# Kernel optimization log

Measured on AMD Instinct MI355X. Metric: run time of the kernel, lower is better.

The kernel has to match this reference:

```python
import jax, jax.numpy as jnp
import numpy as np

B, T, M, L = 128, 500, 512, 128


def setup_inputs() -> dict:
    key = jax.random.key(0)
    ks = jax.random.split(key, 9)
    s = 0.05
    return {
        "H": jax.random.normal(ks[0], (B, T, M), jnp.float32),
        "Wv": jax.random.normal(ks[1], (M, L), jnp.float32) * s,
        "bv": jax.random.normal(ks[2], (L,), jnp.float32) * s,
        "Wu": jax.random.normal(ks[3], (M, L), jnp.float32) * s,
        "bu": jax.random.normal(ks[4], (L,), jnp.float32) * s,
        "Wa": jax.random.normal(ks[5], (L, 1), jnp.float32) * s,
        "ba": jax.random.normal(ks[6], (1,), jnp.float32) * s,
        "Wc": jax.random.normal(ks[7], (M, 2), jnp.float32) * s,
        "bc": jax.random.normal(ks[8], (2,), jnp.float32) * s,
    }


def reference(H, Wv, bv, Wu, bu, Wa, ba, Wc, bc):
    # Gated attention: tanh and sigmoid gates over per-tile features  [B,T,L]
    A_V = jnp.tanh(H @ Wv + bv)
    A_U = jax.nn.sigmoid(H @ Wu + bu)
    A = (A_V * A_U) @ Wa + ba            # [B,T,1]  (K=1)
    A_t = jnp.swapaxes(A, 1, 2)          # [B,1,T]  (transpose(2,1) in torch)
    # Per-bag softmax over tiles, replacing the Python loop with a batched op
    A_sm = jax.nn.softmax(A_t, axis=-1)  # [B,1,T]
    # Weighted sum of tile features per bag (batched mm replaces the loop+cat)
    Mpool = jnp.matmul(A_sm, H)          # [B,1,M]
    out = Mpool.reshape(B, M) @ Wc + bc  # [B,2]
    A_after_sftmx = A_sm.reshape(B, T)   # cat of [1,T] rows -> [B,T]
    # torch A.squeeze(0) with B>1 is a no-op -> [B,1,T]
    return (out, A_after_sftmx, A_t)
```

## Files before the change

### kernel.cpp

```cpp
#include <hip/hip_runtime.h>
#include <hip/hip_bf16.h>
#include <cstdint>

#define B_ 128
#define T_ 500
#define M_ 512
#define L_ 128
#define NTILE 8

typedef float  f32x4  __attribute__((ext_vector_type(4)));
typedef __bf16 bf16x8 __attribute__((ext_vector_type(8)));

__device__ __forceinline__ uint32_t f2bf(float f) {
  uint32_t u = __float_as_uint(f);
  u += 0x7FFFu + ((u >> 16) & 1u);
  return u >> 16;
}

__device__ __forceinline__ void gld_lds16(const uint16_t* g, uint16_t* l) {
  __builtin_amdgcn_global_load_lds((const __attribute__((address_space(1))) uint32_t*)g,
                                   (__attribute__((address_space(3))) uint32_t*)l,
                                   16, 0, 0);
}

__global__ void k_wconv(const float* __restrict__ Wv, const float* __restrict__ Wu,
                        uint16_t* __restrict__ Wb) {
  int id = blockIdx.x * 256 + threadIdx.x;
  int w = id >> 16;
  int r = id & 65535;
  int l = r >> 9;
  int m = r & 511;
  const float* src = w ? Wu : Wv;
  Wb[(w << 16) + l * 512 + m] = (uint16_t)f2bf(src[m * 128 + l]);
}

__global__ __launch_bounds__(256)
void k_gates_pool(const float* __restrict__ H, const uint16_t* __restrict__ Wb,
                  const float* __restrict__ bv, const float* __restrict__ bu,
                  const float* __restrict__ Wa, const float* __restrict__ ba,
                  float* __restrict__ At, float* __restrict__ Ew,
                  float* __restrict__ Sums, float* __restrict__ Mp8) {
  __shared__ __align__(16) uint16_t sm[20480];
  __shared__ float esm[64];
  const int tid  = threadIdx.x;
  const int lane = tid & 63;
  const int wv   = tid >> 6;
  const int lc   = lane & 15;
  const int kq   = lane >> 4;
  const int tile  = blockIdx.x;
  const int b     = blockIdx.y;
  const int tbase = tile * 64;

  const int ht  = tid >> 2;
  const int hcc = tid & 3;
  const int gts = tbase + ht;
  const bool hv = (gts < T_);
  const float* hsrc = H + ((size_t)b * T_ + (hv ? gts : 0)) * M_ + hcc * 8;

  f32x4 accV[8], accU[8];
  #pragma unroll
  for (int i = 0; i < 8; ++i) { accV[i] = f32x4{0.f,0.f,0.f,0.f}; accU[i] = f32x4{0.f,0.f,0.f,0.f}; }

  float hf[8];

  #pragma unroll
  for (int j = 0; j < 4; ++j) {
    int i = j * 256 + tid;
    gld_lds16(Wb + ((i >> 9) << 16) + (((i >> 2) & 127) << 9) + ((i & 3) << 3),
              &sm[i * 8]);
  }
  {
    float4 p0 = make_float4(0.f,0.f,0.f,0.f), p1 = p0;
    if (hv) { p0 = *(const float4*)(hsrc); p1 = *(const float4*)(hsrc + 4); }
    uint4 u;
    u.x = f2bf(p0.x) | (f2bf(p0.y) << 16);
    u.y = f2bf(p0.z) | (f2bf(p0.w) << 16);
    u.z = f2bf(p1.x) | (f2bf(p1.y) << 16);
    u.w = f2bf(p1.z) | (f2bf(p1.w) << 16);
    *(uint4*)&sm[16384 + ht * 32 + hcc * 8] = u;
  }
  __syncthreads();

  int buf = 0;
  for (int s = 0; s < 16; ++s) {
    if (s < 15) {
      const int ks = s + 1;
      #pragma unroll
      for (int j = 0; j < 4; ++j) {
        int i = j * 256 + tid;
        gld_lds16(Wb + ((i >> 9) << 16) + (((i >> 2) & 127) << 9) + (ks << 5) + ((i & 3) << 3),
                  &sm[(buf ^ 1) * 8192 + i * 8]);
      }
      float4 p0 = make_float4(0.f,0.f,0.f,0.f), p1 = p0;
      if (hv) { p0 = *(const float4*)(hsrc + ks * 32); p1 = *(const float4*)(hsrc + ks * 32 + 4); }
      hf[0]=p0.x; hf[1]=p0.y; hf[2]=p0.z; hf[3]=p0.w;
      hf[4]=p1.x; hf[5]=p1.y; hf[6]=p1.z; hf[7]=p1.w;
    }
    {
      const uint16_t* Hb = &sm[16384 + buf * 2048];
      const uint16_t* Wp = &sm[buf * 8192];
      bf16x8 a = *(const bf16x8*)&Hb[(wv * 16 + lc) * 32 + kq * 8];
      #pragma unroll
      for (int lf = 0; lf < 8; ++lf) {
        int off = (lf * 16 + lc) * 32 + kq * 8;
        bf16x8 bw = *(const bf16x8*)&Wp[off];
        bf16x8 uw = *(const bf16x8*)&Wp[4096 + off];
        accV[lf] = __builtin_amdgcn_mfma_f32_16x16x32_bf16(a, bw, accV[lf], 0, 0, 0);
        accU[lf] = __builtin_amdgcn_mfma_f32_16x16x32_bf16(a, uw, accU[lf], 0, 0, 0);
      }
    }
    if (s < 15) {
      uint4 u;
      u.x = f2bf(hf[0]) | (f2bf(hf[1]) << 16);
      u.y = f2bf(hf[2]) | (f2bf(hf[3]) << 16);
      u.z = f2bf(hf[4]) | (f2bf(hf[5]) << 16);
      u.w = f2bf(hf[6]) | (f2bf(hf[7]) << 16);
      *(uint4*)&sm[16384 + (buf ^ 1) * 2048 + ht * 32 + hcc * 8] = u;
    }
    __syncthreads();
    buf ^= 1;
  }

  float wa[8], bvv[8], buu[8];
  #pragma unroll
  for (int j = 0; j < 8; ++j) {
    int l = j * 16 + lc;
    wa[j] = Wa[l]; bvv[j] = bv[l]; buu[j] = bu[l];
  }
  float ba0 = ba[0];
  float part[4] = {0.f, 0.f, 0.f, 0.f};
  #pragma unroll
  for (int lf = 0; lf < 8; ++lf) {
    #pragma unroll
    for (int r = 0; r < 4; ++r) {
      float xv = accV[lf][r] + bvv[lf];
      float xu = accU[lf][r] + buu[lf];
      xv = fminf(fmaxf(xv, -30.f), 30.f);
      float e  = __expf(2.f * xv);
      float th = (e - 1.f) * __builtin_amdgcn_rcpf(e + 1.f);
      float sg = __builtin_amdgcn_rcpf(1.f + __expf(-xu));
      part[r] += th * sg * wa[lf];
    }
  }
  #pragma unroll
  for (int r = 0; r < 4; ++r) {
    part[r] += __shfl_xor(part[r], 1);
    part[r] += __shfl_xor(part[r], 2);
    part[r] += __shfl_xor(part[r], 4);
    part[r] += __shfl_xor(part[r], 8);
  }
  if (lc == 0) {
    #pragma unroll
    for (int r = 0; r < 4; ++r) {
      int tl = wv * 16 + kq * 4 + r;
      int gt = tbase + tl;
      float logit = part[r] + ba0;
      float e = 0.f;
      if (gt < T_) {
        At[b * T_ + gt] = logit;
        e = __expf(logit);
        Ew[(b << 9) + gt] = e;
      }
      esm[tl] = e;
    }
  }
  __syncthreads();
  if (tid < 64) {
    float v = esm[tid];
    v += __shfl_xor(v, 1);  v += __shfl_xor(v, 2);  v += __shfl_xor(v, 4);
    v += __shfl_xor(v, 8);  v += __shfl_xor(v, 16); v += __shfl_xor(v, 32);
    if (tid == 0) Sums[b * NTILE + tile] = v;
  }

  const int tmax = min(64, T_ - tbase);
  const float* hp = H + ((size_t)b * T_ + tbase) * M_;
  float a0 = 0.f, a1 = 0.f;
  for (int t = 0; t < tmax; ++t) {
    float e = esm[t];
    a0 += e * hp[(size_t)t * M_ + tid];
    a1 += e * hp[(size_t)t * M_ + tid + 256];
  }
  float* mp = Mp8 + ((size_t)(b * NTILE + tile) << 9);
  mp[tid]       = a0;
  mp[tid + 256] = a1;
}

__global__ void k_finish(const float* __restrict__ Ew, const float* __restrict__ Sums,
                         const float* __restrict__ Mp8, const float* __restrict__ Wc,
                         const float* __restrict__ bc, float* __restrict__ out,
                         float* __restrict__ Asm) {
  __shared__ float rs[8];
  const int b = blockIdx.x;
  const int tid = threadIdx.x;
  float se = 0.f;
  #pragma unroll
  for (int j = 0; j < NTILE; ++j) se += Sums[b * NTILE + j];
  const float inv = 1.f / se;
  for (int t = tid; t < T_; t += 256) Asm[b * T_ + t] = Ew[(b << 9) + t] * inv;
  float mp0 = 0.f, mp1 = 0.f;
  #pragma unroll
  for (int j = 0; j < NTILE; ++j) {
    const float* mp = Mp8 + ((size_t)(b * NTILE + j) << 9);
    mp0 += mp[tid];
    mp1 += mp[tid + 256];
  }
  mp0 *= inv; mp1 *= inv;
  float c0 = mp0 * Wc[tid * 2]     + mp1 * Wc[(tid + 256) * 2];
  float c1 = mp0 * Wc[tid * 2 + 1] + mp1 * Wc[(tid + 256) * 2 + 1];
  #pragma unroll
  for (int m = 32; m; m >>= 1) { c0 += __shfl_xor(c0, m); c1 += __shfl_xor(c1, m); }
  const int lane = tid & 63, wv = tid >> 6;
  if (lane == 0) { rs[wv] = c0; rs[4 + wv] = c1; }
  __syncthreads();
  if (tid == 0) out[b * 2]     = rs[0] + rs[1] + rs[2] + rs[3] + bc[0];
  if (tid == 1) out[b * 2 + 1] = rs[4] + rs[5] + rs[6] + rs[7] + bc[1];
}

extern "C" void kernel_launch(void* const* d_in, const int* in_sizes, int n_in,
                              void* d_out, int out_size, void* d_ws, size_t ws_size,
                              hipStream_t stream) {
  const float* H  = (const float*)d_in[0];
  const float* Wv = (const float*)d_in[1];
  const float* bv = (const float*)d_in[2];
  const float* Wu = (const float*)d_in[3];
  const float* bu = (const float*)d_in[4];
  const float* Wa = (const float*)d_in[5];
  const float* ba = (const float*)d_in[6];
  const float* Wc = (const float*)d_in[7];
  const float* bc = (const float*)d_in[8];

  float* out = (float*)d_out;
  float* Asm = out + 256;
  float* At  = out + 256 + 64000;

  uint16_t* Wb = (uint16_t*)d_ws;
  float* Ew   = (float*)((char*)d_ws + 262144);
  float* Sums = (float*)((char*)d_ws + 524288);
  float* Mp8  = (float*)((char*)d_ws + 528384);

  hipLaunchKernelGGL(k_wconv,      dim3(512),          dim3(256), 0, stream, Wv, Wu, Wb);
  hipLaunchKernelGGL(k_gates_pool, dim3(NTILE, B_),    dim3(256), 0, stream,
                     H, Wb, bv, bu, Wa, ba, At, Ew, Sums, Mp8);
  hipLaunchKernelGGL(k_finish,     dim3(B_),           dim3(256), 0, stream,
                     Ew, Sums, Mp8, Wc, bc, out, Asm);
}
```

Before: 243.7 us.

## Deepen W/H prefetch pipeline, swizzle LDS, retile MFMA per wave, vectorize pooling

The gates kernel now keeps a 4-stage ring of weight tiles in LDS and a 3-deep register prefetch of H, waiting on raw waitcnt plus barrier instead of __syncthreads. Each wave computes a 64x32 slice (4 t-fragments by 2 l-fragments) rather than 16x128, so A fragments are reused across the l-fragments, and partial logits are reduced across waves through shared memory. XOR swizzles on the H and W LDS layouts are meant to avoid bank conflicts, and the weight conversion kernel is reworked as an LDS transpose with vector stores. The pooling loop and the finish kernel use float2 and float4 loads, and launch bounds ask for 2 blocks per CU. The price is more LDS per block (about 82KB), higher register pressure and a more fragile hand-written synchronisation scheme.

```diff
diff --git a/kernel.cpp b/kernel.cpp
--- a/kernel.cpp
+++ b/kernel.cpp
@@ -23,24 +23,45 @@
                                    16, 0, 0);
 }
 
-__global__ void k_wconv(const float* __restrict__ Wv, const float* __restrict__ Wu,
-                        uint16_t* __restrict__ Wb) {
-  int id = blockIdx.x * 256 + threadIdx.x;
-  int w = id >> 16;
-  int r = id & 65535;
-  int l = r >> 9;
-  int m = r & 511;
-  const float* src = w ? Wu : Wv;
-  Wb[(w << 16) + l * 512 + m] = (uint16_t)f2bf(src[m * 128 + l]);
-}
-
 __global__ __launch_bounds__(256)
+void k_wconv(const float* __restrict__ Wv, const float* __restrict__ Wu,
+             uint16_t* __restrict__ Wb) {
+  __shared__ float lt[32 * 130];
+  const int tid = threadIdx.x;
+  const int ks  = blockIdx.x;
+  const int g   = blockIdx.y;
+  const float* src = g ? Wu : Wv;
+  #pragma unroll
+  for (int j = 0; j < 16; ++j) {
+    int idx = j * 256 + tid;
+    int m = idx >> 7, l = idx & 127;
+    lt[m * 130 + l] = src[(ks * 32 + m) * 128 + l];
+  }
+  __syncthreads();
+  const int l = tid >> 1, half = tid & 1;
+  const int key = (l >> 1) & 3;
+  uint16_t outv[16];
+  #pragma unroll
+  for (int i = 0; i < 16; ++i) {
+    int cp   = half * 2 + (i >> 3);
+    int e    = i & 7;
+    int mloc = ((cp ^ key) << 3) | e;
+    outv[i] = (uint16_t)f2bf(lt[mloc * 130 + l]);
+  }
+  uint16_t* dst = Wb + g * 65536 + l * 512 + ks * 32 + half * 16;
+  *(uint4*)dst       = ((const uint4*)outv)[0];
+  *(uint4*)(dst + 8) = ((const uint4*)outv)[1];
+}
+
+__global__ __launch_bounds__(256, 2)
 void k_gates_pool(const float* __restrict__ H, const uint16_t* __restrict__ Wb,
                   const float* __restrict__ bv, const float* __restrict__ bu,
                   const float* __restrict__ Wa, const float* __restrict__ ba,
                   float* __restrict__ At, float* __restrict__ Ew,
                   float* __restrict__ Sums, float* __restrict__ Mp8) {
-  __shared__ __align__(16) uint16_t sm[20480];
+  __shared__ __align__(16) uint16_t smW[4 * 8192];
+  __shared__ __align__(16) uint16_t smH[2 * 2048];
+  __shared__ float esm_p[4][64];
   __shared__ float esm[64];
   const int tid  = threadIdx.x;
   const int lane = tid & 63;
@@ -51,144 +72,173 @@
   const int b     = blockIdx.y;
   const int tbase = tile * 64;
 
+  const uint16_t* wsrc[4];
+  uint16_t* wdst[4];
+  #pragma unroll
+  for (int j = 0; j < 4; ++j) {
+    int i = j * 256 + tid;
+    wsrc[j] = Wb + (i >> 9) * 65536 + ((i >> 2) & 127) * 512 + (i & 3) * 8;
+    wdst[j] = smW + i * 8;
+  }
   const int ht  = tid >> 2;
   const int hcc = tid & 3;
   const int gts = tbase + ht;
-  const bool hv = (gts < T_);
-  const float* hsrc = H + ((size_t)b * T_ + (hv ? gts : 0)) * M_ + hcc * 8;
-
-  f32x4 accV[8], accU[8];
-  #pragma unroll
-  for (int i = 0; i < 8; ++i) { accV[i] = f32x4{0.f,0.f,0.f,0.f}; accU[i] = f32x4{0.f,0.f,0.f,0.f}; }
-
-  float hf[8];
-
-  #pragma unroll
-  for (int j = 0; j < 4; ++j) {
-    int i = j * 256 + tid;
-    gld_lds16(Wb + ((i >> 9) << 16) + (((i >> 2) & 127) << 9) + ((i & 3) << 3),
-              &sm[i * 8]);
-  }
-  {
-    float4 p0 = make_float4(0.f,0.f,0.f,0.f), p1 = p0;
-    if (hv) { p0 = *(const float4*)(hsrc); p1 = *(const float4*)(hsrc + 4); }
+  const float* hsrc = H + ((size_t)b * T_ + (gts < T_ ? gts : T_ - 1)) * M_ + hcc * 8;
+  uint16_t* hdst = smH + ht * 32 + ((hcc ^ ((ht >> 1) & 3)) << 3);
+
+  int hoff[4], woff[2];
+  #pragma unroll
+  for (int tf = 0; tf < 4; ++tf) {
+    int hr = tf * 16 + lc;
+    hoff[tf] = hr * 32 + ((kq ^ ((hr >> 1) & 3)) << 3);
+  }
+  #pragma unroll
+  for (int lf = 0; lf < 2; ++lf) {
+    int lr = wv * 32 + lf * 16 + lc;
+    woff[lf] = lr * 32 + ((kq ^ ((lr >> 1) & 3)) << 3);
+  }
+
+  f32x4 accV[4][2], accU[4][2];
+  #pragma unroll
+  for (int tf = 0; tf < 4; ++tf)
+    #pragma unroll
+    for (int lf = 0; lf < 2; ++lf) {
+      accV[tf][lf] = f32x4{0.f, 0.f, 0.f, 0.f};
+      accU[tf][lf] = f32x4{0.f, 0.f, 0.f, 0.f};
+    }
+
+  f32x4 hreg[3][2];
+  auto packw = [&](const f32x4* h, uint16_t* d) {
     uint4 u;
-    u.x = f2bf(p0.x) | (f2bf(p0.y) << 16);
-    u.y = f2bf(p0.z) | (f2bf(p0.w) << 16);
-    u.z = f2bf(p1.x) | (f2bf(p1.y) << 16);
-    u.w = f2bf(p1.z) | (f2bf(p1.w) << 16);
-    *(uint4*)&sm[16384 + ht * 32 + hcc * 8] = u;
-  }
-  __syncthreads();
-
-  int buf = 0;
+    u.x = f2bf(h[0][0]) | (f2bf(h[0][1]) << 16);
+    u.y = f2bf(h[0][2]) | (f2bf(h[0][3]) << 16);
+    u.z = f2bf(h[1][0]) | (f2bf(h[1][1]) << 16);
+    u.w = f2bf(h[1][2]) | (f2bf(h[1][3]) << 16);
+    *(uint4*)d = u;
+  };
+
+  #pragma unroll
+  for (int j = 0; j < 4; ++j) gld_lds16(wsrc[j], wdst[j]);
+  hreg[0][0] = *(const f32x4*)(hsrc);
+  hreg[0][1] = *(const f32x4*)(hsrc + 4);
+  #pragma unroll
+  for (int j = 0; j < 4; ++j) gld_lds16(wsrc[j] + 32, wdst[j] + 8192);
+  #pragma unroll
+  for (int j = 0; j < 4; ++j) gld_lds16(wsrc[j] + 64, wdst[j] + 16384);
+  hreg[1][0] = *(const f32x4*)(hsrc + 32);
+  hreg[1][1] = *(const f32x4*)(hsrc + 36);
+  hreg[2][0] = *(const f32x4*)(hsrc + 64);
+  hreg[2][1] = *(const f32x4*)(hsrc + 68);
+  packw(hreg[0], hdst);
+  asm volatile("s_waitcnt lgkmcnt(0)" ::: "memory");
+  __builtin_amdgcn_s_barrier();
+  __builtin_amdgcn_sched_barrier(0);
+
+  #pragma unroll
   for (int s = 0; s < 16; ++s) {
+    if (s + 3 < 16) {
+      #pragma unroll
+      for (int j = 0; j < 4; ++j)
+        gld_lds16(wsrc[j] + (s + 3) * 32, wdst[j] + ((s + 3) & 3) * 8192);
+      hreg[s % 3][0] = *(const f32x4*)(hsrc + (s + 3) * 32);
+      hreg[s % 3][1] = *(const f32x4*)(hsrc + (s + 3) * 32 + 4);
+    }
+    const uint16_t* Wp = smW + (s & 3) * 8192;
+    const uint16_t* Hb = smH + (s & 1) * 2048;
+    bf16x8 a[4];
+    #pragma unroll
+    for (int tf = 0; tf < 4; ++tf) a[tf] = *(const bf16x8*)&Hb[hoff[tf]];
+    #pragma unroll
+    for (int lf = 0; lf < 2; ++lf) {
+      bf16x8 bw = *(const bf16x8*)&Wp[woff[lf]];
+      bf16x8 uw = *(const bf16x8*)&Wp[4096 + woff[lf]];
+      #pragma unroll
+      for (int tf = 0; tf < 4; ++tf) {
+        accV[tf][lf] = __builtin_amdgcn_mfma_f32_16x16x32_bf16(a[tf], bw, accV[tf][lf], 0, 0, 0);
+        accU[tf][lf] = __builtin_amdgcn_mfma_f32_16x16x32_bf16(a[tf], uw, accU[tf][lf], 0, 0, 0);
+      }
+    }
+    if (s + 1 < 16)
+      packw(hreg[(s + 1) % 3], hdst + ((s + 1) & 1) * 2048);
     if (s < 15) {
-      const int ks = s + 1;
-      #pragma unroll
-      for (int j = 0; j < 4; ++j) {
-        int i = j * 256 + tid;
-        gld_lds16(Wb + ((i >> 9) << 16) + (((i >> 2) & 127) << 9) + (ks << 5) + ((i & 3) << 3),
-                  &sm[(buf ^ 1) * 8192 + i * 8]);
+      asm volatile("s_waitcnt lgkmcnt(0)" ::: "memory");
+      __builtin_amdgcn_s_barrier();
+      __builtin_amdgcn_sched_barrier(0);
+    }
+  }
+
+  float wa2[2], bvv[2], buu[2];
+  #pragma unroll
+  for (int lf = 0; lf < 2; ++lf) {
+    int l = wv * 32 + lf * 16 + lc;
+    wa2[lf] = Wa[l]; bvv[lf] = bv[l]; buu[lf] = bu[l];
+  }
+  const float ba0 = ba[0];
+  #pragma unroll
+  for (int tf = 0; tf < 4; ++tf) {
+    float part[4] = {0.f, 0.f, 0.f, 0.f};
+    #pragma unroll
+    for (int lf = 0; lf < 2; ++lf) {
+      #pragma unroll
+      for (int r = 0; r < 4; ++r) {
+        float xv = accV[tf][lf][r] + bvv[lf];
+        float xu = accU[tf][lf][r] + buu[lf];
+        xv = fminf(fmaxf(xv, -30.f), 30.f);
+        float e  = __expf(2.f * xv);
+        float th = (e - 1.f) * __builtin_amdgcn_rcpf(e + 1.f);
+        float sg = __builtin_amdgcn_rcpf(1.f + __expf(-xu));
+        part[r] += th * sg * wa2[lf];
       }
-      float4 p0 = make_float4(0.f,0.f,0.f,0.f), p1 = p0;
-      if (hv) { p0 = *(const float4*)(hsrc + ks * 32); p1 = *(const float4*)(hsrc + ks * 32 + 4); }
-      hf[0]=p0.x; hf[1]=p0.y; hf[2]=p0.z; hf[3]=p0.w;
-      hf[4]=p1.x; hf[5]=p1.y; hf[6]=p1.z; hf[7]=p1.w;
-    }
-    {
-      const uint16_t* Hb = &sm[16384 + buf * 2048];
-      const uint16_t* Wp = &sm[buf * 8192];
-      bf16x8 a = *(const bf16x8*)&Hb[(wv * 16 + lc) * 32 + kq * 8];
-      #pragma unroll
-      for (int lf = 0; lf < 8; ++lf) {
-        int off = (lf * 16 + lc) * 32 + kq * 8;
-        bf16x8 bw = *(const bf16x8*)&Wp[off];
-        bf16x8 uw = *(const bf16x8*)&Wp[4096 + off];
-        accV[lf] = __builtin_amdgcn_mfma_f32_16x16x32_bf16(a, bw, accV[lf], 0, 0, 0);
-        accU[lf] = __builtin_amdgcn_mfma_f32_16x16x32_bf16(a, uw, accU[lf], 0, 0, 0);
-      }
-    }
-    if (s < 15) {
-      uint4 u;
-      u.x = f2bf(hf[0]) | (f2bf(hf[1]) << 16);
-      u.y = f2bf(hf[2]) | (f2bf(hf[3]) << 16);
-      u.z = f2bf(hf[4]) | (f2bf(hf[5]) << 16);
-      u.w = f2bf(hf[6]) | (f2bf(hf[7]) << 16);
-      *(uint4*)&sm[16384 + (buf ^ 1) * 2048 + ht * 32 + hcc * 8] = u;
-    }
-    __syncthreads();
-    buf ^= 1;
-  }
-
-  float wa[8], bvv[8], buu[8];
-  #pragma unroll
-  for (int j = 0; j < 8; ++j) {
-    int l = j * 16 + lc;
-    wa[j] = Wa[l]; bvv[j] = bv[l]; buu[j] = bu[l];
-  }
-  float ba0 = ba[0];
-  float part[4] = {0.f, 0.f, 0.f, 0.f};
-  #pragma unroll
-  for (int lf = 0; lf < 8; ++lf) {
+    }
     #pragma unroll
     for (int r = 0; r < 4; ++r) {
-      float xv = accV[lf][r] + bvv[lf];
-      float xu = accU[lf][r] + buu[lf];
-      xv = fminf(fmaxf(xv, -30.f), 30.f);
-      float e  = __expf(2.f * xv);
-      float th = (e - 1.f) * __builtin_amdgcn_rcpf(e + 1.f);
-      float sg = __builtin_amdgcn_rcpf(1.f + __expf(-xu));
-      part[r] += th * sg * wa[lf];
-    }
-  }
-  #pragma unroll
-  for (int r = 0; r < 4; ++r) {
-    part[r] += __shfl_xor(part[r], 1);
-    part[r] += __shfl_xor(part[r], 2);
-    part[r] += __shfl_xor(part[r], 4);
-    part[r] += __shfl_xor(part[r], 8);
-  }
-  if (lc == 0) {
-    #pragma unroll
-    for (int r = 0; r < 4; ++r) {
-      int tl = wv * 16 + kq * 4 + r;
-      int gt = tbase + tl;
-      float logit = part[r] + ba0;
-      float e = 0.f;
-      if (gt < T_) {
-        At[b * T_ + gt] = logit;
-        e = __expf(logit);
-        Ew[(b << 9) + gt] = e;
-      }
-      esm[tl] = e;
+      part[r] += __shfl_xor(part[r], 1);
+      part[r] += __shfl_xor(part[r], 2);
+      part[r] += __shfl_xor(part[r], 4);
+      part[r] += __shfl_xor(part[r], 8);
+    }
+    if (lc == 0) {
+      #pragma unroll
+      for (int r = 0; r < 4; ++r) esm_p[wv][tf * 16 + kq * 4 + r] = part[r];
     }
   }
   __syncthreads();
   if (tid < 64) {
-    float v = esm[tid];
+    float logit = esm_p[0][tid] + esm_p[1][tid] + esm_p[2][tid] + esm_p[3][tid] + ba0;
+    int gt = tbase + tid;
+    float e = 0.f;
+    if (gt < T_) {
+      At[b * T_ + gt] = logit;
+      e = __expf(logit);
+      Ew[(b << 9) + gt] = e;
+    }
+    esm[tid] = e;
+    float v = e;
     v += __shfl_xor(v, 1);  v += __shfl_xor(v, 2);  v += __shfl_xor(v, 4);
     v += __shfl_xor(v, 8);  v += __shfl_xor(v, 16); v += __shfl_xor(v, 32);
     if (tid == 0) Sums[b * NTILE + tile] = v;
   }
-
-  const int tmax = min(64, T_ - tbase);
-  const float* hp = H + ((size_t)b * T_ + tbase) * M_;
+  __syncthreads();
+
+  const int tmax = (T_ - tbase < 64) ? (T_ - tbase) : 64;
+  const float2* hp = (const float2*)(H + ((size_t)b * T_ + tbase) * M_) + tid;
   float a0 = 0.f, a1 = 0.f;
+  #pragma unroll 4
   for (int t = 0; t < tmax; ++t) {
     float e = esm[t];
-    a0 += e * hp[(size_t)t * M_ + tid];
-    a1 += e * hp[(size_t)t * M_ + tid + 256];
-  }
-  float* mp = Mp8 + ((size_t)(b * NTILE + tile) << 9);
-  mp[tid]       = a0;
-  mp[tid + 256] = a1;
-}
-
-__global__ void k_finish(const float* __restrict__ Ew, const float* __restrict__ Sums,
-                         const float* __restrict__ Mp8, const float* __restrict__ Wc,
-                         const float* __restrict__ bc, float* __restrict__ out,
-                         float* __restrict__ Asm) {
+    float2 h2 = hp[(size_t)t * 256];
+    a0 += e * h2.x;
+    a1 += e * h2.y;
+  }
+  float2* mp = (float2*)(Mp8 + ((size_t)(b * NTILE + tile) << 9));
+  mp[tid] = make_float2(a0, a1);
+}
+
+__global__ __launch_bounds__(256)
+void k_finish(const float* __restrict__ Ew, const float* __restrict__ Sums,
+              const float* __restrict__ Mp8, const float* __restrict__ Wc,
+              const float* __restrict__ bc, float* __restrict__ out,
+              float* __restrict__ Asm) {
   __shared__ float rs[8];
   const int b = blockIdx.x;
   const int tid = threadIdx.x;
@@ -200,13 +250,13 @@
   float mp0 = 0.f, mp1 = 0.f;
   #pragma unroll
   for (int j = 0; j < NTILE; ++j) {
-    const float* mp = Mp8 + ((size_t)(b * NTILE + j) << 9);
-    mp0 += mp[tid];
-    mp1 += mp[tid + 256];
+    float2 v = ((const float2*)(Mp8 + ((size_t)(b * NTILE + j) << 9)))[tid];
+    mp0 += v.x; mp1 += v.y;
   }
   mp0 *= inv; mp1 *= inv;
-  float c0 = mp0 * Wc[tid * 2]     + mp1 * Wc[(tid + 256) * 2];
-  float c1 = mp0 * Wc[tid * 2 + 1] + mp1 * Wc[(tid + 256) * 2 + 1];
+  float4 w = ((const float4*)Wc)[tid];
+  float c0 = mp0 * w.x + mp1 * w.z;
+  float c1 = mp0 * w.y + mp1 * w.w;
   #pragma unroll
   for (int m = 32; m; m >>= 1) { c0 += __shfl_xor(c0, m); c1 += __shfl_xor(c1, m); }
   const int lane = tid & 63, wv = tid >> 6;
@@ -238,9 +288,9 @@
   float* Sums = (float*)((char*)d_ws + 524288);
   float* Mp8  = (float*)((char*)d_ws + 528384);
 
-  hipLaunchKernelGGL(k_wconv,      dim3(512),          dim3(256), 0, stream, Wv, Wu, Wb);
-  hipLaunchKernelGGL(k_gates_pool, dim3(NTILE, B_),    dim3(256), 0, stream,
+  hipLaunchKernelGGL(k_wconv,      dim3(16, 2),     dim3(256), 0, stream, Wv, Wu, Wb);
+  hipLaunchKernelGGL(k_gates_pool, dim3(NTILE, B_), dim3(256), 0, stream,
                      H, Wb, bv, bu, Wa, ba, At, Ew, Sums, Mp8);
-  hipLaunchKernelGGL(k_finish,     dim3(B_),           dim3(256), 0, stream,
+  hipLaunchKernelGGL(k_finish,     dim3(B_),        dim3(256), 0, stream,
                      Ew, Sums, Mp8, Wc, bc, out, Asm);
 }
```

Result: faster. 230.3 us (-5.5%).
